# Kernel tuning notes

Measured on AMD Instinct MI355X. Metric: run time of the kernel, lower is better.

The kernel has to match this reference:

```python
import jax, jax.numpy as jnp
import numpy as np

EPS = 1e-5

def conv2d(x, w, b=None, pad=1):
    y = jax.lax.conv_general_dilated(x, w, (1, 1), ((pad, pad), (pad, pad)),
                                     dimension_numbers=('NCHW', 'OIHW', 'NCHW'))
    if b is not None:
        y = y + b[None, :, None, None]
    return y

def batchnorm(x, g, b):
    # torch training-mode BN: per-channel batch mean / biased variance
    m = x.mean((0, 2, 3), keepdims=True)
    v = ((x - m) ** 2).mean((0, 2, 3), keepdims=True)
    return (x - m) * jax.lax.rsqrt(v + EPS) * g[None, :, None, None] + b[None, :, None, None]

def deform_conv(x, offset, w):
    # x: [B,C,H,W]; offset: [B,2*K*K,H,W] as (dy,dx) pairs per kernel tap; w: [O,C,K,K]
    B, C, H, W = x.shape
    O = w.shape[0]
    K = w.shape[-1]
    off = offset.reshape(B, K * K, 2, H, W)
    ki = jnp.arange(K)
    ky, kx = jnp.meshgrid(ki, ki, indexing='ij')
    ky = ky.reshape(-1).astype(x.dtype)  # [K*K]
    kx = kx.reshape(-1).astype(x.dtype)
    gy = jnp.arange(H, dtype=x.dtype)[None, None, :, None]
    gx = jnp.arange(W, dtype=x.dtype)[None, None, None, :]
    pad = (K - 1) // 2  # stride=1, pad=1, dilation=1
    py = gy + (ky - pad)[None, :, None, None] + off[:, :, 0]  # [B,K*K,H,W]
    px = gx + (kx - pad)[None, :, None, None] + off[:, :, 1]
    y0 = jnp.floor(py)
    x0 = jnp.floor(px)
    wy = py - y0
    wx = px - x0
    y0i = y0.astype(jnp.int32)
    x0i = x0.astype(jnp.int32)
    xf = x.reshape(B, C, H * W)

    def corner(yc, xc):
        valid = ((yc >= 0) & (yc < H) & (xc >= 0) & (xc < W)).astype(x.dtype)
        idx = jnp.clip(yc, 0, H - 1) * W + jnp.clip(xc, 0, W - 1)  # [B,K*K,H,W]
        g = jax.vmap(lambda im, ix: im[:, ix])(xf, idx)  # [B,C,K*K,H,W]
        return g * valid[:, None]

    v00 = corner(y0i, x0i)
    v01 = corner(y0i, x0i + 1)
    v10 = corner(y0i + 1, x0i)
    v11 = corner(y0i + 1, x0i + 1)
    wy_ = wy[:, None]
    wx_ = wx[:, None]
    samp = (v00 * (1 - wy_) * (1 - wx_) + v01 * (1 - wy_) * wx_
            + v10 * wy_ * (1 - wx_) + v11 * wy_ * wx_)  # [B,C,K*K,H,W]
    return jnp.einsum('bckhw,ock->bohw', samp, w.reshape(O, C, K * K))


def setup_inputs() -> dict:
    key = jax.random.key(0)
    ks = jax.random.split(key, 20)
    B, inC, H, W = 64, 3, 64, 64
    G = 1  # num_deformable_groups

    def u(k, shape, fan):
        s = 1.0 / np.sqrt(fan)
        return jax.random.uniform(k, shape, jnp.float32, -s, s)

    return {
        'x':   jax.random.normal(ks[0], (B, inC, H, W), jnp.float32),
        'w1':  u(ks[1], (8, inC, 3, 3), inC * 9),
        'g1':  jnp.ones((8,), jnp.float32),  'b1': jnp.zeros((8,), jnp.float32),
        'w2':  u(ks[2], (20, 8, 3, 3), 8 * 9), 'bc2': u(ks[3], (20,), 8 * 9),
        'g2':  jnp.ones((20,), jnp.float32), 'b2': jnp.zeros((20,), jnp.float32),
        'w3':  u(ks[4], (G * 18, 20, 3, 3), 20 * 9),
        'wd1': u(ks[5], (40, 20, 3, 3), 20 * 9),
        'g3':  jnp.ones((40,), jnp.float32), 'b3': jnp.zeros((40,), jnp.float32),
        'w4':  u(ks[6], (G * 18, 40, 3, 3), 40 * 9), 'bc4': u(ks[7], (G * 18,), 40 * 9),
        'wd2': u(ks[8], (64, 40, 3, 3), 40 * 9),
        'g4':  jnp.ones((64,), jnp.float32), 'b4': jnp.zeros((64,), jnp.float32),
        'fw':  u(ks[9], (10, 256), 256), 'fb': u(ks[10], (10,), 256),
    }


def reference(x, w1, g1, b1, w2, bc2, g2, b2, w3, wd1, g3, b3, w4, bc4, wd2, g4, b4, fw, fb):
    h = batchnorm(jax.nn.relu(conv2d(x, w1)), g1, b1)
    h = batchnorm(jax.nn.relu(conv2d(h, w2, bc2)), g2, b2)
    off1 = conv2d(h, w3)
    h = batchnorm(jax.nn.relu(deform_conv(h, off1, wd1)), g3, b3)
    off2 = conv2d(h, w4, bc4)
    h = batchnorm(jax.nn.relu(deform_conv(h, off2, wd2)), g4, b4)
    em = h
    B, C, H, W = h.shape
    # avg_pool2d kernel [H//2, W//2] (stride defaults to kernel) -> 2x2 output
    p = h.reshape(B, C, 2, H // 2, 2, W // 2).mean(axis=(3, 5))  # [B,C,2,2]
    logits = p.reshape(B, -1) @ fw.T + fb  # [B,10]
    return jax.nn.softmax(logits, axis=-1), em
```

## Files before the change

kernel.cpp:

```cpp
#include <hip/hip_runtime.h>

#define IMW 64
#define HW 4096
#define BATCH 64
#define NPIX (BATCH * HW)
#define TPB 512
#define PIXBLK 8

__device__ inline float bfbits(unsigned int hi16) {
    union { unsigned int i; float f; } v; v.i = hi16; return v.f;
}
__device__ inline float bf_lo(unsigned int u) { return bfbits(u << 16); }
__device__ inline float bf_hi(unsigned int u) { return bfbits(u & 0xffff0000u); }
__device__ inline unsigned short f2bf(float f) {
    union { float f; unsigned int i; } v; v.f = f;
    unsigned int i = v.i;
    i += 0x7fff + ((i >> 16) & 1);
    return (unsigned short)(i >> 16);
}

__device__ inline unsigned pack_h2(float a, float b) {
    union { unsigned u; _Float16 h[2]; } v;
    v.h[0] = (_Float16)a;
    v.h[1] = (_Float16)b;
    return v.u;
}
__device__ inline float h_lo(unsigned u) {
    union { unsigned u; _Float16 h[2]; } v; v.u = u; return (float)v.h[0];
}
__device__ inline float h_hi(unsigned u) {
    union { unsigned u; _Float16 h[2]; } v; v.u = u; return (float)v.h[1];
}

template <int CO_BLOCKS>
__device__ inline void swz(int lin, int& img, int& xblk, int& cob) {
    const int per_img = PIXBLK * CO_BLOCKS;
    int xcd = lin & 7;
    int s = lin >> 3;
    img = xcd * 8 + s / per_img;
    int r = s % per_img;
    cob = r / PIXBLK;
    xblk = r % PIXBLK;
}

template <int CIN, int COUT, bool RELU, bool BIAS, bool AFF, bool IN_NCHW,
          bool IN_BF16, int OUT_MODE>
__global__ void conv3x3_k(const void* __restrict__ in_,
                          const float* __restrict__ w,
                          const float* __restrict__ bias,
                          const float* __restrict__ iscale,
                          const float* __restrict__ ishift,
                          void* __restrict__ out_) {
    __shared__ float lw[9 * CIN * COUT];
    __shared__ float lb[COUT];
    __shared__ float lsc[CIN];
    __shared__ float lsh[CIN];

    for (int dst = threadIdx.x; dst < 9 * CIN * COUT; dst += blockDim.x) {
        int co = dst % COUT;
        int kci = dst / COUT;
        int k = kci / CIN;
        int ci = kci % CIN;
        lw[dst] = w[(size_t)co * (CIN * 9) + ci * 9 + k];
    }
    if (threadIdx.x < COUT) lb[threadIdx.x] = BIAS ? bias[threadIdx.x] : 0.f;
    if (AFF && threadIdx.x < CIN) {
        lsc[threadIdx.x] = iscale[threadIdx.x];
        lsh[threadIdx.x] = ishift[threadIdx.x];
    }
    __syncthreads();

    int img, xblk, cob;
    swz<1>(blockIdx.x, img, xblk, cob);
    int b = img;
    int pos = xblk * TPB + threadIdx.x;
    int p = (b << 12) + pos;
    int y = pos >> 6;
    int x = pos & 63;

    float acc[COUT];
#pragma unroll
    for (int co = 0; co < COUT; ++co) acc[co] = lb[co];

#pragma unroll 1
    for (int k = 0; k < 9; ++k) {
        int ky = k / 3, kx = k - ky * 3;
        int yy = y + ky - 1, xx = x + kx - 1;
        if (yy < 0 || yy >= IMW || xx < 0 || xx >= IMW) continue;

        float vin[CIN];
        if constexpr (IN_NCHW) {
            const float* ip = (const float*)in_;
#pragma unroll
            for (int ci = 0; ci < CIN; ++ci)
                vin[ci] = ip[((size_t)(b * CIN + ci) << 12) + yy * IMW + xx];
        } else if constexpr (!IN_BF16) {
            const float* ip = (const float*)in_ + ((size_t)((b << 12) + yy * IMW + xx)) * CIN;
#pragma unroll
            for (int c4 = 0; c4 < CIN / 4; ++c4) {
                float4 v = *(const float4*)(ip + c4 * 4);
                vin[c4 * 4 + 0] = v.x;
                vin[c4 * 4 + 1] = v.y;
                vin[c4 * 4 + 2] = v.z;
                vin[c4 * 4 + 3] = v.w;
            }
        } else if constexpr (CIN % 8 == 0) {
            const uint4* ip = (const uint4*)((const unsigned short*)in_ +
                                             ((size_t)((b << 12) + yy * IMW + xx)) * CIN);
#pragma unroll
            for (int c8 = 0; c8 < CIN / 8; ++c8) {
                uint4 u = ip[c8];
                vin[c8 * 8 + 0] = bf_lo(u.x); vin[c8 * 8 + 1] = bf_hi(u.x);
                vin[c8 * 8 + 2] = bf_lo(u.y); vin[c8 * 8 + 3] = bf_hi(u.y);
                vin[c8 * 8 + 4] = bf_lo(u.z); vin[c8 * 8 + 5] = bf_hi(u.z);
                vin[c8 * 8 + 6] = bf_lo(u.w); vin[c8 * 8 + 7] = bf_hi(u.w);
            }
        } else {
            const uint2* ip = (const uint2*)((const unsigned short*)in_ +
                                             ((size_t)((b << 12) + yy * IMW + xx)) * CIN);
#pragma unroll
            for (int c4 = 0; c4 < CIN / 4; ++c4) {
                uint2 u = ip[c4];
                vin[c4 * 4 + 0] = bf_lo(u.x); vin[c4 * 4 + 1] = bf_hi(u.x);
                vin[c4 * 4 + 2] = bf_lo(u.y); vin[c4 * 4 + 3] = bf_hi(u.y);
            }
        }
        if constexpr (AFF) {
#pragma unroll
            for (int ci = 0; ci < CIN; ++ci)
                vin[ci] = fmaf(vin[ci], lsc[ci], lsh[ci]);
        }
#pragma unroll
        for (int ci = 0; ci < CIN; ++ci) {
            float s = vin[ci];
            const float* wr = &lw[(k * CIN + ci) * COUT];
#pragma unroll
            for (int co = 0; co < COUT; ++co)
                acc[co] = fmaf(wr[co], s, acc[co]);
        }
    }

    if (RELU) {
#pragma unroll
        for (int co = 0; co < COUT; ++co) acc[co] = fmaxf(acc[co], 0.f);
    }

    if constexpr (OUT_MODE == 2) {
        unsigned* o = (unsigned*)out_;
#pragma unroll
        for (int i = 0; i < COUT / 2; ++i)
            o[(size_t)i * NPIX + p] = pack_h2(acc[2 * i], acc[2 * i + 1]);
    } else if constexpr (OUT_MODE == 1) {
        unsigned int us[COUT / 2];
#pragma unroll
        for (int i = 0; i < COUT / 2; ++i)
            us[i] = (unsigned int)f2bf(acc[2 * i]) | ((unsigned int)f2bf(acc[2 * i + 1]) << 16);
        uint2* o2 = (uint2*)((unsigned short*)out_ + (size_t)p * COUT);
#pragma unroll
        for (int i = 0; i < COUT / 4; ++i)
            o2[i] = make_uint2(us[2 * i], us[2 * i + 1]);
    } else {
        float* op = (float*)out_ + (size_t)p * COUT;
        if constexpr (COUT % 4 == 0) {
#pragma unroll
            for (int c4 = 0; c4 < COUT / 4; ++c4)
                *(float4*)(op + c4 * 4) =
                    make_float4(acc[c4 * 4], acc[c4 * 4 + 1], acc[c4 * 4 + 2], acc[c4 * 4 + 3]);
        } else {
#pragma unroll
            for (int c2 = 0; c2 < COUT / 2; ++c2)
                *(float2*)(op + c2 * 2) = make_float2(acc[c2 * 2], acc[c2 * 2 + 1]);
        }
    }
}

template <int CIN, int COUT_TOT, int COUT_BLK, int CO_BLOCKS, bool OUT_NCHW>
__global__ void deform_k(const void* __restrict__ in_,
                         const unsigned* __restrict__ off,
                         const float* __restrict__ w,
                         const float* __restrict__ iscale,
                         const float* __restrict__ ishift,
                         void* __restrict__ out_) {
    __shared__ float lw[9 * CIN * COUT_BLK];
    __shared__ float lsc[CIN];
    __shared__ float lsh[CIN];

    int img, xblk, cob;
    swz<CO_BLOCKS>(blockIdx.x, img, xblk, cob);
    int co_base = cob * COUT_BLK;

    for (int dst = threadIdx.x; dst < 9 * CIN * COUT_BLK; dst += blockDim.x) {
        int co = dst % COUT_BLK;
        int kci = dst / COUT_BLK;
        int k = kci / CIN;
        int ci = kci % CIN;
        lw[dst] = w[(size_t)(co_base + co) * (CIN * 9) + ci * 9 + k];
    }
    if (threadIdx.x < CIN) {
        lsc[threadIdx.x] = iscale[threadIdx.x];
        lsh[threadIdx.x] = ishift[threadIdx.x];
    }
    __syncthreads();

    int b = img;
    int pos = xblk * TPB + threadIdx.x;
    int p = (b << 12) + pos;
    int y = pos >> 6;
    int x = pos & 63;

    float acc[COUT_BLK];
#pragma unroll
    for (int co = 0; co < COUT_BLK; ++co) acc[co] = 0.f;

    unsigned od[9];
#pragma unroll
    for (int j = 0; j < 9; ++j) od[j] = off[(size_t)j * NPIX + p];

    const unsigned short* ib = (const unsigned short*)in_ + (size_t)b * HW * CIN;

#pragma unroll 1
    for (int k = 0; k < 9; ++k) {
        int ky = k / 3, kx = k - ky * 3;
        float py = (float)(y + ky - 1) + h_lo(od[k]);
        float px = (float)(x + kx - 1) + h_hi(od[k]);
        float fy = floorf(py), fx = floorf(px);
        float wy = py - fy, wx = px - fx;
        int y0 = (int)fy, x0 = (int)fx;
        int y1 = y0 + 1, x1 = x0 + 1;
        bool vy0 = (unsigned)y0 < (unsigned)IMW;
        bool vy1 = (unsigned)y1 < (unsigned)IMW;
        bool vx0 = (unsigned)x0 < (unsigned)IMW;
        bool vx1 = (unsigned)x1 < (unsigned)IMW;
        int cy0 = min(max(y0, 0), IMW - 1), cy1 = min(max(y1, 0), IMW - 1);
        int cx0 = min(max(x0, 0), IMW - 1), cx1 = min(max(x1, 0), IMW - 1);
        float w00 = (1.f - wy) * (1.f - wx) * ((vy0 & vx0) ? 1.f : 0.f);
        float w01 = (1.f - wy) * wx * ((vy0 & vx1) ? 1.f : 0.f);
        float w10 = wy * (1.f - wx) * ((vy1 & vx0) ? 1.f : 0.f);
        float w11 = wy * wx * ((vy1 & vx1) ? 1.f : 0.f);
        float wsum = w00 + w01 + w10 + w11;

        if constexpr (CIN % 8 == 0) {
            const uint4* q00 = (const uint4*)(ib + (size_t)(cy0 * IMW + cx0) * CIN);
            const uint4* q01 = (const uint4*)(ib + (size_t)(cy0 * IMW + cx1) * CIN);
            const uint4* q10 = (const uint4*)(ib + (size_t)(cy1 * IMW + cx0) * CIN);
            const uint4* q11 = (const uint4*)(ib + (size_t)(cy1 * IMW + cx1) * CIN);
#pragma unroll
            for (int c8 = 0; c8 < CIN / 8; ++c8) {
                uint4 a = q00[c8], bq = q01[c8], c = q10[c8], d = q11[c8];
#pragma unroll
                for (int h = 0; h < 4; ++h) {
                    unsigned int ua = (&a.x)[h], ub = (&bq.x)[h];
                    unsigned int uc = (&c.x)[h], ud = (&d.x)[h];
                    int ci0 = c8 * 8 + h * 2;
                    float r0 = w00 * bf_lo(ua) + w01 * bf_lo(ub) +
                               w10 * bf_lo(uc) + w11 * bf_lo(ud);
                    float r1 = w00 * bf_hi(ua) + w01 * bf_hi(ub) +
                               w10 * bf_hi(uc) + w11 * bf_hi(ud);
                    float s0 = fmaf(r0, lsc[ci0], lsh[ci0] * wsum);
                    float s1 = fmaf(r1, lsc[ci0 + 1], lsh[ci0 + 1] * wsum);
                    const float* wr0 = &lw[(k * CIN + ci0) * COUT_BLK];
                    const float* wr1 = &lw[(k * CIN + ci0 + 1) * COUT_BLK];
#pragma unroll
                    for (int co = 0; co < COUT_BLK; ++co)
                        acc[co] = fmaf(wr0[co], s0, acc[co]);
#pragma unroll
                    for (int co = 0; co < COUT_BLK; ++co)
                        acc[co] = fmaf(wr1[co], s1, acc[co]);
                }
            }
        } else {
            const uint2* q00 = (const uint2*)(ib + (size_t)(cy0 * IMW + cx0) * CIN);
            const uint2* q01 = (const uint2*)(ib + (size_t)(cy0 * IMW + cx1) * CIN);
            const uint2* q10 = (const uint2*)(ib + (size_t)(cy1 * IMW + cx0) * CIN);
            const uint2* q11 = (const uint2*)(ib + (size_t)(cy1 * IMW + cx1) * CIN);
#pragma unroll
            for (int c4 = 0; c4 < CIN / 4; ++c4) {
                uint2 a = q00[c4], bq = q01[c4], c = q10[c4], d = q11[c4];
#pragma unroll
                for (int h = 0; h < 2; ++h) {
                    unsigned int ua = (&a.x)[h], ub = (&bq.x)[h];
                    unsigned int uc = (&c.x)[h], ud = (&d.x)[h];
                    int ci0 = c4 * 4 + h * 2;
                    float r0 = w00 * bf_lo(ua) + w01 * bf_lo(ub) +
                               w10 * bf_lo(uc) + w11 * bf_lo(ud);
                    float r1 = w00 * bf_hi(ua) + w01 * bf_hi(ub) +
                               w10 * bf_hi(uc) + w11 * bf_hi(ud);
                    float s0 = fmaf(r0, lsc[ci0], lsh[ci0] * wsum);
                    float s1 = fmaf(r1, lsc[ci0 + 1], lsh[ci0 + 1] * wsum);
                    const float* wr0 = &lw[(k * CIN + ci0) * COUT_BLK];
                    const float* wr1 = &lw[(k * CIN + ci0 + 1) * COUT_BLK];
#pragma unroll
                    for (int co = 0; co < COUT_BLK; ++co)
                        acc[co] = fmaf(wr0[co], s0, acc[co]);
#pragma unroll
                    for (int co = 0; co < COUT_BLK; ++co)
                        acc[co] = fmaf(wr1[co], s1, acc[co]);
                }
            }
        }
    }

#pragma unroll
    for (int co = 0; co < COUT_BLK; ++co) acc[co] = fmaxf(acc[co], 0.f);

    if constexpr (OUT_NCHW) {
        float* o = (float*)out_;
#pragma unroll
        for (int co = 0; co < COUT_BLK; ++co)
            __builtin_nontemporal_store(acc[co],
                &o[((size_t)(b * COUT_TOT + co_base + co) << 12) + pos]);
    } else {
        unsigned int us[COUT_BLK / 2];
#pragma unroll
        for (int i = 0; i < COUT_BLK / 2; ++i)
            us[i] = (unsigned int)f2bf(acc[2 * i]) | ((unsigned int)f2bf(acc[2 * i + 1]) << 16);
        unsigned short* ob = (unsigned short*)out_ + (size_t)p * COUT_TOT + co_base;
        if constexpr (COUT_BLK % 8 == 0) {
            uint4* o4 = (uint4*)ob;
#pragma unroll
            for (int i = 0; i < COUT_BLK / 8; ++i)
                o4[i] = make_uint4(us[4 * i], us[4 * i + 1], us[4 * i + 2], us[4 * i + 3]);
        } else {
            uint2* o2 = (uint2*)ob;
#pragma unroll
            for (int i = 0; i < COUT_BLK / 4; ++i)
                o2[i] = make_uint2(us[2 * i], us[2 * i + 1]);
        }
    }
}

template <int C>
__global__ void bn_partial_nhwc(const float* __restrict__ src, float* __restrict__ sums) {
    const size_t total = (size_t)NPIX * C;
    size_t stride = (size_t)gridDim.x * blockDim.x;
    float s = 0.f, q = 0.f;
    for (size_t i = (size_t)blockIdx.x * blockDim.x + threadIdx.x; i < total; i += stride) {
        float v = src[i];
        s += v;
        q += v * v;
    }
    __shared__ float ls[320], lq[320];
    ls[threadIdx.x] = s;
    lq[threadIdx.x] = q;
    __syncthreads();
    if (threadIdx.x < C) {
        float a = 0.f, bb = 0.f;
        for (int j = threadIdx.x; j < 320; j += C) {
            a += ls[j];
            bb += lq[j];
        }
        atomicAdd(&sums[threadIdx.x], a);
        atomicAdd(&sums[C + threadIdx.x], bb);
    }
}

template <int C>
__global__ void bn_partial_nhwc_bf16(const unsigned short* __restrict__ src,
                                     float* __restrict__ sums) {
    const int CP = C / 2;
    const size_t totalu = (size_t)NPIX * CP;
    const unsigned int* s32 = (const unsigned int*)src;
    size_t stride = (size_t)gridDim.x * blockDim.x;
    float s0 = 0.f, q0 = 0.f, s1 = 0.f, q1 = 0.f;
    for (size_t i = (size_t)blockIdx.x * blockDim.x + threadIdx.x; i < totalu; i += stride) {
        unsigned int u = s32[i];
        float a = bf_lo(u), b = bf_hi(u);
        s0 += a; q0 += a * a;
        s1 += b; q1 += b * b;
    }
    __shared__ float l0[320], m0[320], l1[320], m1[320];
    l0[threadIdx.x] = s0; m0[threadIdx.x] = q0;
    l1[threadIdx.x] = s1; m1[threadIdx.x] = q1;
    __syncthreads();
    if (threadIdx.x < C) {
        int cp = threadIdx.x >> 1, hi = threadIdx.x & 1;
        float a = 0.f, bb = 0.f;
        for (int j = cp; j < 320; j += CP) {
            a += hi ? l1[j] : l0[j];
            bb += hi ? m1[j] : m0[j];
        }
        atomicAdd(&sums[threadIdx.x], a);
        atomicAdd(&sums[C + threadIdx.x], bb);
    }
}

__global__ void bn_partial_nchw(const float* __restrict__ src, int C, int parts,
                                float* __restrict__ sums) {
    int c = blockIdx.x / parts;
    int part = blockIdx.x % parts;
    int chunk = NPIX / parts;
    int start = part * chunk;
    float s = 0.f, q = 0.f;
    for (int i = start + threadIdx.x; i < start + chunk; i += blockDim.x) {
        int bb = i >> 12, pos = i & 4095;
        float v = src[((size_t)(bb * C + c) << 12) + pos];
        s += v;
        q += v * v;
    }
    __shared__ float ls[256], lq[256];
    ls[threadIdx.x] = s;
    lq[threadIdx.x] = q;
    __syncthreads();
    for (int st = 128; st > 0; st >>= 1) {
        if (threadIdx.x < st) {
            ls[threadIdx.x] += ls[threadIdx.x + st];
            lq[threadIdx.x] += lq[threadIdx.x + st];
        }
        __syncthreads();
    }
    if (threadIdx.x == 0) {
        atomicAdd(&sums[c], ls[0]);
        atomicAdd(&sums[C + c], lq[0]);
    }
}

__global__ void bn_finalize_kernel(const float* __restrict__ sums, int C,
                                   const float* __restrict__ g,
                                   const float* __restrict__ b,
                                   float* __restrict__ scale,
                                   float* __restrict__ shift) {
    int c = threadIdx.x;
    if (c >= C) return;
    const float invN = 1.f / (float)NPIX;
    float mean = sums[c] * invN;
    float var = sums[C + c] * invN - mean * mean;
    float sc = g[c] * rsqrtf(var + 1e-5f);
    scale[c] = sc;
    shift[c] = b[c] - mean * sc;
}

__global__ void bn4_apply_pool(float* __restrict__ em,
                               const float* __restrict__ scale,
                               const float* __restrict__ shift,
                               float* __restrict__ pw) {
    int bc = blockIdx.x;
    int c = bc & 63;
    int t = threadIdx.x;
    float sc = scale[c], sh = shift[c];
    float* base = em + ((size_t)bc << 12);
    int pos = t * 16;
    int quad = ((pos >= 2048) ? 2 : 0) + ((pos & 63) >> 5);
    float s = 0.f;
#pragma unroll
    for (int k4 = 0; k4 < 4; ++k4) {
        float4 v = *(float4*)(base + pos + k4 * 4);
        v.x = fmaf(v.x, sc, sh);
        v.y = fmaf(v.y, sc, sh);
        v.z = fmaf(v.z, sc, sh);
        v.w = fmaf(v.w, sc, sh);
        *(float4*)(base + pos + k4 * 4) = v;
        s += v.x + v.y + v.z + v.w;
    }
    __shared__ float qs[4];
    if (t < 4) qs[t] = 0.f;
    __syncthreads();
    atomicAdd(&qs[quad], s);
    __syncthreads();
    if (t < 4) pw[bc * 4 + t] = qs[t] * (1.f / 1024.f);
}

__global__ void fc_softmax_kernel(const float* __restrict__ pw,
                                  const float* __restrict__ fw,
                                  const float* __restrict__ fb,
                                  float* __restrict__ out) {
    int b = blockIdx.x;
    int t = threadIdx.x;
    __shared__ float logits[10];
    if (t < 10) {
        float acc = fb[t];
        const float* p = pw + b * 256;
        for (int q = 0; q < 256; ++q) acc = fmaf(p[q], fw[t * 256 + q], acc);
        logits[t] = acc;
    }
    __syncthreads();
    if (t == 0) {
        float m = -1e30f;
        for (int q = 0; q < 10; ++q) m = fmaxf(m, logits[q]);
        float e[10], sum = 0.f;
        for (int q = 0; q < 10; ++q) { e[q] = expf(logits[q] - m); sum += e[q]; }
        float inv = 1.f / sum;
        for (int q = 0; q < 10; ++q) out[b * 10 + q] = e[q] * inv;
    }
}

extern "C" void kernel_launch(void* const* d_in, const int* in_sizes, int n_in,
                              void* d_out, int out_size, void* d_ws, size_t ws_size,
                              hipStream_t stream) {
    (void)in_sizes; (void)n_in; (void)out_size; (void)ws_size;

    const float* x   = (const float*)d_in[0];
    const float* w1  = (const float*)d_in[1];
    const float* g1  = (const float*)d_in[2];
    const float* b1  = (const float*)d_in[3];
    const float* w2  = (const float*)d_in[4];
    const float* bc2 = (const float*)d_in[5];
    const float* g2  = (const float*)d_in[6];
    const float* b2  = (const float*)d_in[7];
    const float* w3  = (const float*)d_in[8];
    const float* wd1 = (const float*)d_in[9];
    const float* g3  = (const float*)d_in[10];
    const float* b3  = (const float*)d_in[11];
    const float* w4  = (const float*)d_in[12];
    const float* bc4 = (const float*)d_in[13];
    const float* wd2 = (const float*)d_in[14];
    const float* g4  = (const float*)d_in[15];
    const float* b4  = (const float*)d_in[16];
    const float* fw  = (const float*)d_in[17];
    const float* fb  = (const float*)d_in[18];

    float* out = (float*)d_out;
    float* softout = out;
    float* em = out + 640;

    float* ws = (float*)d_ws;
    float* h1 = ws;
    unsigned short* h2b = (unsigned short*)(h1 + (size_t)2097152);
    unsigned short* h3b = h2b + (size_t)5242880;
    unsigned* offu = (unsigned*)(h3b + (size_t)10485760);
    float* sums = (float*)(offu + (size_t)9 * NPIX);
    float* scale = sums + 128;
    float* shift = scale + 64;
    float* pw = shift + 64;

    dim3 blk(TPB);
    dim3 gpix(BATCH * PIXBLK);

    conv3x3_k<3, 8, true, false, false, true, false, 0>
        <<<gpix, blk, 0, stream>>>(x, w1, nullptr, nullptr, nullptr, h1);
    hipMemsetAsync(sums, 0, 128 * sizeof(float), stream);
    bn_partial_nhwc<8><<<256, 320, 0, stream>>>(h1, sums);
    bn_finalize_kernel<<<1, 64, 0, stream>>>(sums, 8, g1, b1, scale, shift);

    conv3x3_k<8, 20, true, true, true, false, false, 1>
        <<<gpix, blk, 0, stream>>>(h1, w2, bc2, scale, shift, h2b);
    hipMemsetAsync(sums, 0, 128 * sizeof(float), stream);
    bn_partial_nhwc_bf16<20><<<256, 320, 0, stream>>>(h2b, sums);
    bn_finalize_kernel<<<1, 64, 0, stream>>>(sums, 20, g2, b2, scale, shift);

    conv3x3_k<20, 18, false, false, true, false, true, 2>
        <<<gpix, blk, 0, stream>>>(h2b, w3, nullptr, scale, shift, offu);
    deform_k<20, 40, 20, 2, false>
        <<<dim3(BATCH * PIXBLK * 2), blk, 0, stream>>>(h2b, offu, wd1, scale, shift, h3b);
    hipMemsetAsync(sums, 0, 128 * sizeof(float), stream);
    bn_partial_nhwc_bf16<40><<<256, 320, 0, stream>>>(h3b, sums);
    bn_finalize_kernel<<<1, 64, 0, stream>>>(sums, 40, g3, b3, scale, shift);

    conv3x3_k<40, 18, false, true, true, false, true, 2>
        <<<gpix, blk, 0, stream>>>(h3b, w4, bc4, scale, shift, offu);
    deform_k<40, 64, 32, 2, true>
        <<<dim3(BATCH * PIXBLK * 2), blk, 0, stream>>>(h3b, offu, wd2, scale, shift, em);
    hipMemsetAsync(sums, 0, 128 * sizeof(float), stream);
    bn_partial_nchw<<<64 * 32, 256, 0, stream>>>(em, 64, 32, sums);
    bn_finalize_kernel<<<1, 64, 0, stream>>>(sums, 64, g4, b4, scale, shift);

    bn4_apply_pool<<<64 * 64, 256, 0, stream>>>(em, scale, shift, pw);
    fc_softmax_kernel<<<64, 64, 0, stream>>>(pw, fw, fb, softout);
}
```

Measured before the change: 686.7 us.

## Double-buffer per-tap deform weights in LDS and vectorize NCHW BN stats

For the second deformable conv, the block no longer stages all nine taps of weights into shared memory. It keeps only two tap slices, loading the next tap while the current one is consumed, with a barrier after each tap. This cuts LDS use from about 46KB to about 10KB per block, which should allow more resident blocks, at the cost of nine extra barriers per block and weight loads spread through the loop. The NCHW batch-norm partial-sum kernel separately switches to float4 loads.

```diff
diff --git a/kernel.cpp b/kernel.cpp
--- a/kernel.cpp
+++ b/kernel.cpp
@@ -174,14 +174,16 @@
     }
 }
 
-template <int CIN, int COUT_TOT, int COUT_BLK, int CO_BLOCKS, bool OUT_NCHW>
+template <int CIN, int COUT_TOT, int COUT_BLK, int CO_BLOCKS, bool OUT_NCHW, bool PERTAP>
 __global__ void deform_k(const void* __restrict__ in_,
                          const unsigned* __restrict__ off,
                          const float* __restrict__ w,
                          const float* __restrict__ iscale,
                          const float* __restrict__ ishift,
                          void* __restrict__ out_) {
-    __shared__ float lw[9 * CIN * COUT_BLK];
+    constexpr int WSLICE = CIN * COUT_BLK;
+    constexpr int LWSZ = PERTAP ? 2 * WSLICE : 9 * WSLICE;
+    __shared__ float lw[LWSZ];
     __shared__ float lsc[CIN];
     __shared__ float lsh[CIN];
 
@@ -189,17 +191,42 @@
     swz<CO_BLOCKS>(blockIdx.x, img, xblk, cob);
     int co_base = cob * COUT_BLK;
 
-    for (int dst = threadIdx.x; dst < 9 * CIN * COUT_BLK; dst += blockDim.x) {
-        int co = dst % COUT_BLK;
-        int kci = dst / COUT_BLK;
-        int k = kci / CIN;
-        int ci = kci % CIN;
-        lw[dst] = w[(size_t)(co_base + co) * (CIN * 9) + ci * 9 + k];
-    }
     if (threadIdx.x < CIN) {
         lsc[threadIdx.x] = iscale[threadIdx.x];
         lsh[threadIdx.x] = ishift[threadIdx.x];
     }
+
+    const float* wsrc = nullptr;
+    if constexpr (PERTAP) {
+        wsrc = w + (size_t)(co_base + (threadIdx.x & (COUT_BLK - 1))) * (CIN * 9) +
+               (threadIdx.x / COUT_BLK) * 9;
+    } else {
+        for (int dst = threadIdx.x; dst < 9 * WSLICE; dst += blockDim.x) {
+            int co = dst % COUT_BLK;
+            int kci = dst / COUT_BLK;
+            int k = kci / CIN;
+            int ci = kci % CIN;
+            lw[dst] = w[(size_t)(co_base + co) * (CIN * 9) + ci * 9 + k];
+        }
+    }
+
+    constexpr int NFULL = WSLICE / TPB;
+    constexpr int REM = WSLICE - NFULL * TPB;
+    constexpr int CISTEP = TPB / COUT_BLK;
+
+    auto stage_tap = [&](int k, int buf) {
+        if constexpr (PERTAP) {
+            const float* src = wsrc + k;
+            float* d = lw + buf * WSLICE + threadIdx.x;
+#pragma unroll
+            for (int j = 0; j < NFULL; ++j)
+                d[j * TPB] = src[(size_t)j * CISTEP * 9];
+            if (REM > 0 && threadIdx.x < REM)
+                d[NFULL * TPB] = src[(size_t)NFULL * CISTEP * 9];
+        }
+    };
+
+    if constexpr (PERTAP) stage_tap(0, 0);
     __syncthreads();
 
     int b = img;
@@ -220,6 +247,11 @@
 
 #pragma unroll 1
     for (int k = 0; k < 9; ++k) {
+        if constexpr (PERTAP) {
+            if (k < 8) stage_tap(k + 1, (k + 1) & 1);
+        }
+        const int kbase = PERTAP ? (k & 1) * CIN : k * CIN;
+
         int ky = k / 3, kx = k - ky * 3;
         float py = (float)(y + ky - 1) + h_lo(od[k]);
         float px = (float)(x + kx - 1) + h_hi(od[k]);
@@ -258,8 +290,8 @@
                                w10 * bf_hi(uc) + w11 * bf_hi(ud);
                     float s0 = fmaf(r0, lsc[ci0], lsh[ci0] * wsum);
                     float s1 = fmaf(r1, lsc[ci0 + 1], lsh[ci0 + 1] * wsum);
-                    const float* wr0 = &lw[(k * CIN + ci0) * COUT_BLK];
-                    const float* wr1 = &lw[(k * CIN + ci0 + 1) * COUT_BLK];
+                    const float* wr0 = &lw[(kbase + ci0) * COUT_BLK];
+                    const float* wr1 = &lw[(kbase + ci0 + 1) * COUT_BLK];
 #pragma unroll
                     for (int co = 0; co < COUT_BLK; ++co)
                         acc[co] = fmaf(wr0[co], s0, acc[co]);
@@ -287,8 +319,8 @@
                                w10 * bf_hi(uc) + w11 * bf_hi(ud);
                     float s0 = fmaf(r0, lsc[ci0], lsh[ci0] * wsum);
                     float s1 = fmaf(r1, lsc[ci0 + 1], lsh[ci0 + 1] * wsum);
-                    const float* wr0 = &lw[(k * CIN + ci0) * COUT_BLK];
-                    const float* wr1 = &lw[(k * CIN + ci0 + 1) * COUT_BLK];
+                    const float* wr0 = &lw[(kbase + ci0) * COUT_BLK];
+                    const float* wr1 = &lw[(kbase + ci0 + 1) * COUT_BLK];
 #pragma unroll
                     for (int co = 0; co < COUT_BLK; ++co)
                         acc[co] = fmaf(wr0[co], s0, acc[co]);
@@ -298,6 +330,8 @@
                 }
             }
         }
+
+        if constexpr (PERTAP) __syncthreads();
     }
 
 #pragma unroll
@@ -391,11 +425,12 @@
     int chunk = NPIX / parts;
     int start = part * chunk;
     float s = 0.f, q = 0.f;
-    for (int i = start + threadIdx.x; i < start + chunk; i += blockDim.x) {
-        int bb = i >> 12, pos = i & 4095;
-        float v = src[((size_t)(bb * C + c) << 12) + pos];
-        s += v;
-        q += v * v;
+    for (int i4 = start / 4 + threadIdx.x; i4 < (start + chunk) / 4; i4 += blockDim.x) {
+        int p4 = i4 * 4;
+        int bb = p4 >> 12, pos = p4 & 4095;
+        float4 v = *(const float4*)&src[((size_t)(bb * C + c) << 12) + pos];
+        s += v.x + v.y + v.z + v.w;
+        q += v.x * v.x + v.y * v.y + v.z * v.z + v.w * v.w;
     }
     __shared__ float ls[256], lq[256];
     ls[threadIdx.x] = s;
@@ -539,7 +574,7 @@
 
     conv3x3_k<20, 18, false, false, true, false, true, 2>
         <<<gpix, blk, 0, stream>>>(h2b, w3, nullptr, scale, shift, offu);
-    deform_k<20, 40, 20, 2, false>
+    deform_k<20, 40, 20, 2, false, false>
         <<<dim3(BATCH * PIXBLK * 2), blk, 0, stream>>>(h2b, offu, wd1, scale, shift, h3b);
     hipMemsetAsync(sums, 0, 128 * sizeof(float), stream);
     bn_partial_nhwc_bf16<40><<<256, 320, 0, stream>>>(h3b, sums);
@@ -547,7 +582,7 @@
 
     conv3x3_k<40, 18, false, true, true, false, true, 2>
         <<<gpix, blk, 0, stream>>>(h3b, w4, bc4, scale, shift, offu);
-    deform_k<40, 64, 32, 2, true>
+    deform_k<40, 64, 32, 2, true, true>
         <<<dim3(BATCH * PIXBLK * 2), blk, 0, stream>>>(h3b, offu, wd2, scale, shift, em);
     hipMemsetAsync(sums, 0, 128 * sizeof(float), stream);
     bn_partial_nchw<<<64 * 32, 256, 0, stream>>>(em, 64, 32, sums);
```

Result: faster. 599.6 us (-12.7%).
